# Performance work log

Measured on AMD Instinct MI355X. Metric: run time of the kernel, lower is better.

The kernel has to match this reference:

```python
import jax, jax.numpy as jnp
import numpy as np

K = 8        # number of nearest neighbors (idw default)
POWER = 2    # inverse-distance power (idw default)
EPS = 1e-8


def setup_inputs() -> dict:
    key = jax.random.key(0)
    kq, kr, kf = jax.random.split(key, 3)
    N, M = 32768, 16384
    # scale coords so points are spread out like real LiDAR scenes
    query_points = jax.random.normal(kq, (N, 3), dtype=jnp.float32) * 10.0
    ref_points = jax.random.normal(kr, (M, 3), dtype=jnp.float32) * 10.0
    ref_flow = jax.random.normal(kf, (M, 3), dtype=jnp.float32)
    return {"query_points": query_points, "ref_points": ref_points, "ref_flow": ref_flow}


def reference(query_points, ref_points, ref_flow):
    # cdist: Euclidean distance [N, M] via (q-r)^2 = |q|^2 + |r|^2 - 2 q.r
    q2 = jnp.sum(query_points * query_points, axis=-1, keepdims=True)      # [N,1]
    r2 = jnp.sum(ref_points * ref_points, axis=-1)                          # [M]
    d2 = q2 + r2 - 2.0 * (query_points @ ref_points.T)                      # [N,M]
    dist = jnp.sqrt(jnp.maximum(d2, 0.0))
    # k smallest distances == top_k of negated distances
    neg_knn, knn_idx = jax.lax.top_k(-dist, K)                               # [N,K]
    knn_dist = -neg_knn
    # inverse-distance weights: 1 / (d^power + eps), normalized over k
    weights = 1.0 / (knn_dist ** POWER + EPS)
    weights = weights / jnp.sum(weights, axis=1, keepdims=True)
    knn_flow = ref_flow[knn_idx]                                             # [N,K,3]
    return jnp.sum(weights[..., None] * knn_flow, axis=1)                    # [N,3]
```

## Files before the change

kernel.cpp:

```cpp
#include <hip/hip_runtime.h>

#define KNN    8
#define BLOCK  256
#define TILE   2048
#define GD     32
#define NC     (GD*GD*GD)
#define EPSW   1e-8f
#define BIGF   3.4e38f

__device__ __forceinline__ void insert8(float d2, int j, float bd[KNN], int bi[KNN]) {
    if (d2 < bd[0]) {
        bd[0] = d2; bi[0] = j;
#pragma unroll
        for (int t = 0; t < KNN - 1; t++) {
            if (bd[t] < bd[t + 1]) {
                float td = bd[t]; bd[t] = bd[t + 1]; bd[t + 1] = td;
                int   ti = bi[t]; bi[t] = bi[t + 1]; bi[t + 1] = ti;
            }
        }
    }
}

__device__ __forceinline__ void ced(float& a, int& ai, float& b, int& bi) {
    if (a < b) { float t = a; a = b; b = t; int ti = ai; ai = bi; bi = ti; }
}
__device__ __forceinline__ void sort8_desc(float d[KNN], int ix[KNN]) {
    ced(d[0],ix[0],d[4],ix[4]); ced(d[1],ix[1],d[5],ix[5]);
    ced(d[2],ix[2],d[6],ix[6]); ced(d[3],ix[3],d[7],ix[7]);
    ced(d[0],ix[0],d[2],ix[2]); ced(d[1],ix[1],d[3],ix[3]);
    ced(d[4],ix[4],d[6],ix[6]); ced(d[5],ix[5],d[7],ix[7]);
    ced(d[0],ix[0],d[1],ix[1]); ced(d[2],ix[2],d[3],ix[3]);
    ced(d[4],ix[4],d[5],ix[5]); ced(d[6],ix[6],d[7],ix[7]);
}
__device__ __forceinline__ void merge_lists(float bd[KNN], int bi[KNN], int mask, bool sort_after) {
    float pd[KNN]; int pi[KNN];
#pragma unroll
    for (int j = 0; j < KNN; j++) { pd[j] = __shfl_xor(bd[j], mask); pi[j] = __shfl_xor(bi[j], mask); }
#pragma unroll
    for (int j = 0; j < KNN; j++) {
        if (pd[KNN - 1 - j] < bd[j]) { bd[j] = pd[KNN - 1 - j]; bi[j] = pi[KNN - 1 - j]; }
    }
    if (sort_after) sort8_desc(bd, bi);
}
__device__ __forceinline__ float merged_thr4(const float bd[KNN]) {
    float c[KNN], p[KNN];
#pragma unroll
    for (int j = 0; j < KNN; j++) c[j] = bd[j];
#pragma unroll
    for (int j = 0; j < KNN; j++) p[j] = __shfl_xor(c[j], 1);
#pragma unroll
    for (int j = 0; j < KNN; j++) c[j] = fminf(c[j], p[KNN - 1 - j]);
    {
        float mx, mn;
        mx = fmaxf(c[0],c[4]); mn = fminf(c[0],c[4]); c[0]=mx; c[4]=mn;
        mx = fmaxf(c[1],c[5]); mn = fminf(c[1],c[5]); c[1]=mx; c[5]=mn;
        mx = fmaxf(c[2],c[6]); mn = fminf(c[2],c[6]); c[2]=mx; c[6]=mn;
        mx = fmaxf(c[3],c[7]); mn = fminf(c[3],c[7]); c[3]=mx; c[7]=mn;
        mx = fmaxf(c[0],c[2]); mn = fminf(c[0],c[2]); c[0]=mx; c[2]=mn;
        mx = fmaxf(c[1],c[3]); mn = fminf(c[1],c[3]); c[1]=mx; c[3]=mn;
        mx = fmaxf(c[4],c[6]); mn = fminf(c[4],c[6]); c[4]=mx; c[6]=mn;
        mx = fmaxf(c[5],c[7]); mn = fminf(c[5],c[7]); c[5]=mx; c[7]=mn;
        mx = fmaxf(c[0],c[1]); mn = fminf(c[0],c[1]); c[0]=mx; c[1]=mn;
        mx = fmaxf(c[2],c[3]); mn = fminf(c[2],c[3]); c[2]=mx; c[3]=mn;
        mx = fmaxf(c[4],c[5]); mn = fminf(c[4],c[5]); c[4]=mx; c[5]=mn;
        mx = fmaxf(c[6],c[7]); mn = fminf(c[6],c[7]); c[6]=mx; c[7]=mn;
    }
#pragma unroll
    for (int j = 0; j < KNN; j++) p[j] = __shfl_xor(c[j], 2);
#pragma unroll
    for (int j = 0; j < KNN; j++) c[j] = fminf(c[j], p[KNN - 1 - j]);
    float m = c[0];
#pragma unroll
    for (int j = 1; j < KNN; j++) m = fmaxf(m, c[j]);
    return m;
}

__device__ __forceinline__ unsigned fenc(float f) {
    unsigned u = __float_as_uint(f);
    return (u & 0x80000000u) ? ~u : (u | 0x80000000u);
}
__device__ __forceinline__ float fdec(unsigned e) {
    unsigned u = (e & 0x80000000u) ? (e ^ 0x80000000u) : ~e;
    return __uint_as_float(u);
}

__device__ __forceinline__ void load_bb(const unsigned* __restrict__ bbw,
                                        float mn[3], float inv[3], float& hmin) {
    hmin = BIGF;
#pragma unroll
    for (int a = 0; a < 3; a++) {
        float lo = fdec(bbw[a]), hi = fdec(bbw[3 + a]);
        float w = fmaxf(hi - lo, 1e-9f);
        mn[a] = lo;
        inv[a] = (float)GD / w;
        hmin = fminf(hmin, w / (float)GD);
    }
}

__device__ __forceinline__ int cell_clamp(int c) {
    return c < 0 ? 0 : (c > GD - 1 ? GD - 1 : c);
}


__global__ __launch_bounds__(256) void bbox_atomic(const float* __restrict__ r, int M,
                                                   unsigned* __restrict__ bbw) {
    float mn0 = BIGF, mn1 = BIGF, mn2 = BIGF;
    float mx0 = -BIGF, mx1 = -BIGF, mx2 = -BIGF;
    for (int j = blockIdx.x * 256 + threadIdx.x; j < M; j += gridDim.x * 256) {
        float x = r[3 * j], y = r[3 * j + 1], z = r[3 * j + 2];
        mn0 = fminf(mn0, x); mx0 = fmaxf(mx0, x);
        mn1 = fminf(mn1, y); mx1 = fmaxf(mx1, y);
        mn2 = fminf(mn2, z); mx2 = fmaxf(mx2, z);
    }
#pragma unroll
    for (int o = 32; o > 0; o >>= 1) {
        mn0 = fminf(mn0, __shfl_xor(mn0, o));
        mn1 = fminf(mn1, __shfl_xor(mn1, o));
        mn2 = fminf(mn2, __shfl_xor(mn2, o));
        mx0 = fmaxf(mx0, __shfl_xor(mx0, o));
        mx1 = fmaxf(mx1, __shfl_xor(mx1, o));
        mx2 = fmaxf(mx2, __shfl_xor(mx2, o));
    }
    if ((threadIdx.x & 63) == 0) {
        atomicMin(bbw + 0, fenc(mn0)); atomicMin(bbw + 1, fenc(mn1)); atomicMin(bbw + 2, fenc(mn2));
        atomicMax(bbw + 3, fenc(mx0)); atomicMax(bbw + 4, fenc(mx1)); atomicMax(bbw + 5, fenc(mx2));
    }
}

__global__ __launch_bounds__(256) void hist2(const float* __restrict__ r,
                                             const float* __restrict__ q,
                                             int M, int N, const unsigned* __restrict__ bbw,
                                             int* __restrict__ rcid, int* __restrict__ qcid,
                                             int* __restrict__ rcnt, int* __restrict__ qcnt) {
    float mn[3], inv[3], hmin;
    load_bb(bbw, mn, inv, hmin);
    int i = blockIdx.x * 256 + threadIdx.x;
    if (i < M) {
        int cx = cell_clamp((int)((r[3 * i]     - mn[0]) * inv[0]));
        int cy = cell_clamp((int)((r[3 * i + 1] - mn[1]) * inv[1]));
        int cz = cell_clamp((int)((r[3 * i + 2] - mn[2]) * inv[2]));
        int cid = (cz * GD + cy) * GD + cx;
        rcid[i] = cid;
        atomicAdd(rcnt + cid, 1);
    } else if (i < M + N) {
        int j = i - M;
        int cx = cell_clamp((int)((q[3 * j]     - mn[0]) * inv[0]));
        int cy = cell_clamp((int)((q[3 * j + 1] - mn[1]) * inv[1]));
        int cz = cell_clamp((int)((q[3 * j + 2] - mn[2]) * inv[2]));
        int cid = (cz * GD + cy) * GD + cx;
        qcid[j] = cid;
        atomicAdd(qcnt + cid, 1);
    }
}

__global__ __launch_bounds__(1024) void scan2(int* __restrict__ rcnt, int* __restrict__ rstart,
                                              int* __restrict__ qcnt, int* __restrict__ qstart) {
    int* cnt = (blockIdx.x == 0) ? rcnt : qcnt;
    int* st  = (blockIdx.x == 0) ? rstart : qstart;
    __shared__ int part[1024];
    int t = threadIdx.x;
    int base = t * 32;
    int s = 0;
#pragma unroll
    for (int k = 0; k < 32; k++) s += cnt[base + k];
    part[t] = s;
    __syncthreads();
    for (int off = 1; off < 1024; off <<= 1) {
        int v = (t >= off) ? part[t - off] : 0;
        __syncthreads();
        part[t] += v;
        __syncthreads();
    }
    int run = part[t] - s;
#pragma unroll
    for (int k = 0; k < 32; k++) {
        int c = cnt[base + k];
        st[base + k] = run;
        cnt[base + k] = run;
        run += c;
    }
    if (t == 1023) st[NC] = run;
}

__global__ __launch_bounds__(256) void scatter2(const float* __restrict__ r, int M, int N,
                                                const int* __restrict__ rcid,
                                                const int* __restrict__ qcid,
                                                int* __restrict__ rcur, int* __restrict__ qcur,
                                                float4* __restrict__ rps, int* __restrict__ sidx,
                                                int* __restrict__ qorder) {
    int i = blockIdx.x * 256 + threadIdx.x;
    if (i < M) {
        int pos = atomicAdd(rcur + rcid[i], 1);
        float x = r[3 * i], y = r[3 * i + 1], z = r[3 * i + 2];
        rps[pos] = make_float4(x, y, z, x * x + y * y + z * z);
        sidx[pos] = i;
    } else if (i < M + N) {
        int j = i - M;
        int pos = atomicAdd(qcur + qcid[j], 1);
        qorder[pos] = j;
    }
}

__global__ __launch_bounds__(256) void knn_pass1(
    const float4* __restrict__ rps, const int* __restrict__ rstart,
    const int* __restrict__ qorder, const float* __restrict__ q,
    const int* __restrict__ sidx, const float* __restrict__ f,
    const unsigned* __restrict__ bbw, float* __restrict__ out,
    int* __restrict__ pend, int* __restrict__ pcnt, int N) {
    int t = blockIdx.x * 256 + threadIdx.x;
    int g = t >> 2;
    int sub = t & 3;
    if (g >= N) return;
    int qi = qorder[g];
    float qx = q[3 * qi], qy = q[3 * qi + 1], qz = q[3 * qi + 2];
    float q2 = qx * qx + qy * qy + qz * qz;
    float mn[3], inv[3], hmin;
    load_bb(bbw, mn, inv, hmin);
    int cx = cell_clamp((int)((qx - mn[0]) * inv[0]));
    int cy = cell_clamp((int)((qy - mn[1]) * inv[1]));
    int cz = cell_clamp((int)((qz - mn[2]) * inv[2]));

    float bd[KNN]; int bi[KNN];
#pragma unroll
    for (int k = 0; k < KNN; k++) { bd[k] = BIGF; bi[k] = 0; }
    float thr = BIGF;

    int rs[9], re[9];
#pragma unroll
    for (int dz = -1; dz <= 1; dz++) {
#pragma unroll
        for (int dy = -1; dy <= 1; dy++) {
            int k = (dz + 1) * 3 + (dy + 1);
            int z = cz + dz, y = cy + dy;
            if ((unsigned)z >= GD || (unsigned)y >= GD) { rs[k] = 0; re[k] = 0; }
            else {
                int rowb = (z * GD + y) * GD;
                int x0 = max(cx - 1, 0), x1 = min(cx + 1, GD - 1);
                rs[k] = rstart[rowb + x0]; re[k] = rstart[rowb + x1 + 1];
            }
        }
    }
#pragma unroll
    for (int k = 0; k < 9; k++) {
        for (int ii = rs[k] + sub; ii < re[k]; ii += 4) {
            float4 p = rps[ii];
            float d2 = (q2 + p.w) - 2.0f * (qx * p.x + qy * p.y + qz * p.z);
            if (d2 < thr) { insert8(d2, ii, bd, bi); thr = bd[0]; }
        }
    }
    float mthr = merged_thr4(bd);
    thr = fminf(thr, mthr);
    bool done = (mthr <= hmin * hmin);

    if (!done) {
        for (int dz = -2; dz <= 2; dz++) {
            int z = cz + dz;
            if ((unsigned)z >= GD) continue;
            for (int dy = -2; dy <= 2; dy++) {
                int y = cy + dy;
                if ((unsigned)y >= GD) continue;
                int rowb = (z * GD + y) * GD;
                if (dz == -2 || dz == 2 || dy == -2 || dy == 2) {
                    int x0 = max(cx - 2, 0), x1 = min(cx + 2, GD - 1);
                    int s = rstart[rowb + x0], e = rstart[rowb + x1 + 1];
                    for (int ii = s + sub; ii < e; ii += 4) {
                        float4 p = rps[ii];
                        float d2 = (q2 + p.w) - 2.0f * (qx * p.x + qy * p.y + qz * p.z);
                        if (d2 < thr) { insert8(d2, ii, bd, bi); thr = bd[0]; }
                    }
                } else {
                    int xl = cx - 2, xr = cx + 2;
                    if (xl >= 0) {
                        int s = rstart[rowb + xl], e = rstart[rowb + xl + 1];
                        for (int ii = s + sub; ii < e; ii += 4) {
                            float4 p = rps[ii];
                            float d2 = (q2 + p.w) - 2.0f * (qx * p.x + qy * p.y + qz * p.z);
                            if (d2 < thr) { insert8(d2, ii, bd, bi); thr = bd[0]; }
                        }
                    }
                    if (xr < GD) {
                        int s = rstart[rowb + xr], e = rstart[rowb + xr + 1];
                        for (int ii = s + sub; ii < e; ii += 4) {
                            float4 p = rps[ii];
                            float d2 = (q2 + p.w) - 2.0f * (qx * p.x + qy * p.y + qz * p.z);
                            if (d2 < thr) { insert8(d2, ii, bd, bi); thr = bd[0]; }
                        }
                    }
                }
            }
        }
        mthr = merged_thr4(bd);
        done = (mthr <= 4.0f * hmin * hmin);
    }

    if (!done) {
        if (sub == 0) { int pos = atomicAdd(pcnt, 1); pend[pos] = qi; }
        return;
    }

    merge_lists(bd, bi, 1, true);
    merge_lists(bd, bi, 2, false);
    if (sub == 0) {
        float wsum = 0.f, ox = 0.f, oy = 0.f, oz = 0.f;
#pragma unroll
        for (int k = 0; k < KNN; k++) {
            float w = 1.0f / (fmaxf(bd[k], 0.0f) + EPSW);
            int j = sidx[bi[k]];
            wsum += w;
            ox += w * f[3 * j];
            oy += w * f[3 * j + 1];
            oz += w * f[3 * j + 2];
        }
        float invw = 1.0f / wsum;
        out[3 * qi]     = ox * invw;
        out[3 * qi + 1] = oy * invw;
        out[3 * qi + 2] = oz * invw;
    }
}

__global__ __launch_bounds__(256) void knn_pass2(
    const float4* __restrict__ rps, const int* __restrict__ pend,
    const int* __restrict__ pcnt, const float* __restrict__ q,
    const int* __restrict__ sidx, const float* __restrict__ f,
    float* __restrict__ out, int M) {
    int lane = threadIdx.x & 63;
    int wid = (blockIdx.x * 256 + threadIdx.x) >> 6;
    int nw = gridDim.x * 4;
    int cnt = *pcnt;
    for (int w = wid; w < cnt; w += nw) {
        int qi = pend[w];
        float qx = q[3 * qi], qy = q[3 * qi + 1], qz = q[3 * qi + 2];
        float q2 = qx * qx + qy * qy + qz * qz;
        float bd[KNN]; int bi[KNN];
#pragma unroll
        for (int k = 0; k < KNN; k++) { bd[k] = BIGF; bi[k] = 0; }
        float thr = BIGF;
        int i = lane;
        for (; i + 192 < M; i += 256) {
            float4 p0 = rps[i];
            float4 p1 = rps[i + 64];
            float4 p2 = rps[i + 128];
            float4 p3 = rps[i + 192];
            float d0 = (q2 + p0.w) - 2.0f * (qx * p0.x + qy * p0.y + qz * p0.z);
            float d1 = (q2 + p1.w) - 2.0f * (qx * p1.x + qy * p1.y + qz * p1.z);
            float d2 = (q2 + p2.w) - 2.0f * (qx * p2.x + qy * p2.y + qz * p2.z);
            float d3 = (q2 + p3.w) - 2.0f * (qx * p3.x + qy * p3.y + qz * p3.z);
            if (d0 < thr) { insert8(d0, i,       bd, bi); thr = bd[0]; }
            if (d1 < thr) { insert8(d1, i + 64,  bd, bi); thr = bd[0]; }
            if (d2 < thr) { insert8(d2, i + 128, bd, bi); thr = bd[0]; }
            if (d3 < thr) { insert8(d3, i + 192, bd, bi); thr = bd[0]; }
        }
        for (; i < M; i += 64) {
            float4 p = rps[i];
            float d2 = (q2 + p.w) - 2.0f * (qx * p.x + qy * p.y + qz * p.z);
            if (d2 < thr) { insert8(d2, i, bd, bi); thr = bd[0]; }
        }
        merge_lists(bd, bi, 1, true);
        merge_lists(bd, bi, 2, true);
        merge_lists(bd, bi, 4, true);
        merge_lists(bd, bi, 8, true);
        merge_lists(bd, bi, 16, true);
        merge_lists(bd, bi, 32, false);
        if (lane == 0) {
            float wsum = 0.f, ox = 0.f, oy = 0.f, oz = 0.f;
#pragma unroll
            for (int k = 0; k < KNN; k++) {
                float wgt = 1.0f / (fmaxf(bd[k], 0.0f) + EPSW);
                int j = sidx[bi[k]];
                wsum += wgt;
                ox += wgt * f[3 * j];
                oy += wgt * f[3 * j + 1];
                oz += wgt * f[3 * j + 2];
            }
            float invw = 1.0f / wsum;
            out[3 * qi]     = ox * invw;
            out[3 * qi + 1] = oy * invw;
            out[3 * qi + 2] = oz * invw;
        }
    }
}

__global__ __launch_bounds__(BLOCK) void knn_fused(
    const float* __restrict__ q, const float* __restrict__ r,
    const float* __restrict__ f, float* __restrict__ out, int N, int M) {
    __shared__ float4 lds[TILE];
    int qi = blockIdx.x * BLOCK + threadIdx.x;
    float qx = 0.f, qy = 0.f, qz = 0.f, q2 = 0.f;
    if (qi < N) {
        qx = q[3 * qi]; qy = q[3 * qi + 1]; qz = q[3 * qi + 2];
        q2 = qx * qx + qy * qy + qz * qz;
    }
    float bd[KNN]; int bi[KNN];
#pragma unroll
    for (int k = 0; k < KNN; k++) { bd[k] = BIGF; bi[k] = 0; }
    for (int tb = 0; tb < M; tb += TILE) {
        int cnt = min(TILE, M - tb);
        for (int i = threadIdx.x; i < cnt; i += BLOCK) {
            int j = tb + i;
            float rx = r[3 * j], ry = r[3 * j + 1], rz = r[3 * j + 2];
            lds[i] = make_float4(rx, ry, rz, rx * rx + ry * ry + rz * rz);
        }
        __syncthreads();
        for (int i = 0; i < cnt; i++) {
            float4 p = lds[i];
            float d2 = (q2 + p.w) - 2.0f * (qx * p.x + qy * p.y + qz * p.z);
            insert8(d2, tb + i, bd, bi);
        }
        __syncthreads();
    }
    if (qi < N) {
        float wsum = 0.f, ox = 0.f, oy = 0.f, oz = 0.f;
#pragma unroll
        for (int k = 0; k < KNN; k++) {
            float w = 1.0f / (fmaxf(bd[k], 0.0f) + EPSW);
            int j = bi[k];
            ox += w * f[3 * j];
            oy += w * f[3 * j + 1];
            oz += w * f[3 * j + 2];
        }
        float inv = 1.0f / wsum;
        out[3 * qi]     = ox * inv;
        out[3 * qi + 1] = oy * inv;
        out[3 * qi + 2] = oz * inv;
    }
}

extern "C" void kernel_launch(void* const* d_in, const int* in_sizes, int n_in,
                              void* d_out, int out_size, void* d_ws, size_t ws_size,
                              hipStream_t stream) {
    const float* q = (const float*)d_in[0];
    const float* r = (const float*)d_in[1];
    const float* f = (const float*)d_in[2];
    float* out = (float*)d_out;
    int N = in_sizes[0] / 3;
    int M = in_sizes[1] / 3;

    size_t off = 0;
    auto take = [&](size_t b) { size_t o = off; off += (b + 255) & ~(size_t)255; return o; };
    size_t o_rps  = take((size_t)M * 16);
    size_t o_sidx = take((size_t)M * 4);
    size_t o_rcid = take((size_t)M * 4);
    size_t o_qcid = take((size_t)N * 4);
    size_t o_qord = take((size_t)N * 4);
    size_t o_rst  = take((size_t)(NC + 1) * 4);
    size_t o_qst  = take((size_t)(NC + 1) * 4);
    size_t o_rcur = take((size_t)NC * 4);
    size_t o_qcur = take((size_t)NC * 4);
    size_t o_pcnt = take(4);
    size_t o_pend = take((size_t)N * 4);
    size_t o_bb   = take(64);

    int grid_x = (N + BLOCK - 1) / BLOCK;
    if (off <= ws_size) {
        char* w = (char*)d_ws;
        float4* rps   = (float4*)(w + o_rps);
        int* sidx     = (int*)(w + o_sidx);
        int* rcid     = (int*)(w + o_rcid);
        int* qcid     = (int*)(w + o_qcid);
        int* qorder   = (int*)(w + o_qord);
        int* rstart   = (int*)(w + o_rst);
        int* qstart   = (int*)(w + o_qst);
        int* rcur     = (int*)(w + o_rcur);
        int* qcur     = (int*)(w + o_qcur);
        int* pcnt     = (int*)(w + o_pcnt);
        int* pend     = (int*)(w + o_pend);
        unsigned* bbw = (unsigned*)(w + o_bb);

        hipMemsetAsync(w + o_rcur, 0, o_pcnt + 4 - o_rcur, stream);
        hipMemsetAsync(w + o_bb, 0xFF, 12, stream);
        hipMemsetAsync(w + o_bb + 12, 0x00, 12, stream);

        int g_all = (M + N + 255) / 256;
        bbox_atomic<<<64, 256, 0, stream>>>(r, M, bbw);
        hist2<<<g_all, 256, 0, stream>>>(r, q, M, N, bbw, rcid, qcid, rcur, qcur);
        scan2<<<2, 1024, 0, stream>>>(rcur, rstart, qcur, qstart);
        scatter2<<<g_all, 256, 0, stream>>>(r, M, N, rcid, qcid, rcur, qcur, rps, sidx, qorder);
        int g_p1 = (int)(((size_t)N * 4 + 255) / 256);
        knn_pass1<<<g_p1, 256, 0, stream>>>(rps, rstart, qorder, q, sidx, f, bbw, out,
                                            pend, pcnt, N);
        knn_pass2<<<512, 256, 0, stream>>>(rps, pend, pcnt, q, sidx, f, out, M);
    } else {
        knn_fused<<<grid_x, BLOCK, 0, stream>>>(q, r, f, out, N, M);
    }
}
```

Before: 225.6 us.

## Add radius-3 shell search, block-wide brute fallback, fold memsets into bbox kernel

Adds a third grid shell (radius 3) before falling back to brute force, so fewer queries reach the costly full scan. The fallback pass now assigns one 256-thread block per pending query instead of one wave, and merges the four per-wave top-8 lists through shared memory. It also replaces two memsets with zeroing inside the bbox kernel and stores the max as a negated min, so a single 0xFF memset initialises all bounds. The costs are more per-query branching and code size in pass1, plus block barriers in pass2.

```diff
diff --git a/kernel.cpp b/kernel.cpp
--- a/kernel.cpp
+++ b/kernel.cpp
@@ -89,7 +89,7 @@
     hmin = BIGF;
 #pragma unroll
     for (int a = 0; a < 3; a++) {
-        float lo = fdec(bbw[a]), hi = fdec(bbw[3 + a]);
+        float lo = fdec(bbw[a]), hi = -fdec(bbw[3 + a]);
         float w = fmaxf(hi - lo, 1e-9f);
         mn[a] = lo;
         inv[a] = (float)GD / w;
@@ -102,11 +102,14 @@
 }
 
 
-__global__ __launch_bounds__(256) void bbox_atomic(const float* __restrict__ r, int M,
-                                                   unsigned* __restrict__ bbw) {
+__global__ __launch_bounds__(256) void bbox_zero(const float* __restrict__ r, int M,
+                                                 unsigned* __restrict__ bbw,
+                                                 int* __restrict__ zbase, int zcount) {
+    int idx = blockIdx.x * 256 + threadIdx.x;
+    for (int j = idx; j < zcount; j += gridDim.x * 256) zbase[j] = 0;
     float mn0 = BIGF, mn1 = BIGF, mn2 = BIGF;
     float mx0 = -BIGF, mx1 = -BIGF, mx2 = -BIGF;
-    for (int j = blockIdx.x * 256 + threadIdx.x; j < M; j += gridDim.x * 256) {
+    for (int j = idx; j < M; j += gridDim.x * 256) {
         float x = r[3 * j], y = r[3 * j + 1], z = r[3 * j + 2];
         mn0 = fminf(mn0, x); mx0 = fmaxf(mx0, x);
         mn1 = fminf(mn1, y); mx1 = fmaxf(mx1, y);
@@ -123,7 +126,7 @@
     }
     if ((threadIdx.x & 63) == 0) {
         atomicMin(bbw + 0, fenc(mn0)); atomicMin(bbw + 1, fenc(mn1)); atomicMin(bbw + 2, fenc(mn2));
-        atomicMax(bbw + 3, fenc(mx0)); atomicMax(bbw + 4, fenc(mx1)); atomicMax(bbw + 5, fenc(mx2));
+        atomicMin(bbw + 3, fenc(-mx0)); atomicMin(bbw + 4, fenc(-mx1)); atomicMin(bbw + 5, fenc(-mx2));
     }
 }
 
@@ -201,6 +204,49 @@
     }
 }
 
+__device__ __forceinline__ void scan_shell(
+    int R, int cx, int cy, int cz, int sub,
+    const float4* __restrict__ rps, const int* __restrict__ rstart,
+    float qx, float qy, float qz, float q2,
+    float bd[KNN], int bi[KNN], float& thr) {
+    for (int dz = -R; dz <= R; ++dz) {
+        int z = cz + dz;
+        if ((unsigned)z >= GD) continue;
+        for (int dy = -R; dy <= R; ++dy) {
+            int y = cy + dy;
+            if ((unsigned)y >= GD) continue;
+            int rowb = (z * GD + y) * GD;
+            if (dz == -R || dz == R || dy == -R || dy == R) {
+                int x0 = max(cx - R, 0), x1 = min(cx + R, GD - 1);
+                int s = rstart[rowb + x0], e = rstart[rowb + x1 + 1];
+                for (int ii = s + sub; ii < e; ii += 4) {
+                    float4 p = rps[ii];
+                    float d2 = (q2 + p.w) - 2.0f * (qx * p.x + qy * p.y + qz * p.z);
+                    if (d2 < thr) { insert8(d2, ii, bd, bi); thr = bd[0]; }
+                }
+            } else {
+                int xl = cx - R, xr = cx + R;
+                if (xl >= 0) {
+                    int s = rstart[rowb + xl], e = rstart[rowb + xl + 1];
+                    for (int ii = s + sub; ii < e; ii += 4) {
+                        float4 p = rps[ii];
+                        float d2 = (q2 + p.w) - 2.0f * (qx * p.x + qy * p.y + qz * p.z);
+                        if (d2 < thr) { insert8(d2, ii, bd, bi); thr = bd[0]; }
+                    }
+                }
+                if (xr < GD) {
+                    int s = rstart[rowb + xr], e = rstart[rowb + xr + 1];
+                    for (int ii = s + sub; ii < e; ii += 4) {
+                        float4 p = rps[ii];
+                        float d2 = (q2 + p.w) - 2.0f * (qx * p.x + qy * p.y + qz * p.z);
+                        if (d2 < thr) { insert8(d2, ii, bd, bi); thr = bd[0]; }
+                    }
+                }
+            }
+        }
+    }
+}
+
 __global__ __launch_bounds__(256) void knn_pass1(
     const float4* __restrict__ rps, const int* __restrict__ rstart,
     const int* __restrict__ qorder, const float* __restrict__ q,
@@ -253,44 +299,15 @@
     bool done = (mthr <= hmin * hmin);
 
     if (!done) {
-        for (int dz = -2; dz <= 2; dz++) {
-            int z = cz + dz;
-            if ((unsigned)z >= GD) continue;
-            for (int dy = -2; dy <= 2; dy++) {
-                int y = cy + dy;
-                if ((unsigned)y >= GD) continue;
-                int rowb = (z * GD + y) * GD;
-                if (dz == -2 || dz == 2 || dy == -2 || dy == 2) {
-                    int x0 = max(cx - 2, 0), x1 = min(cx + 2, GD - 1);
-                    int s = rstart[rowb + x0], e = rstart[rowb + x1 + 1];
-                    for (int ii = s + sub; ii < e; ii += 4) {
-                        float4 p = rps[ii];
-                        float d2 = (q2 + p.w) - 2.0f * (qx * p.x + qy * p.y + qz * p.z);
-                        if (d2 < thr) { insert8(d2, ii, bd, bi); thr = bd[0]; }
-                    }
-                } else {
-                    int xl = cx - 2, xr = cx + 2;
-                    if (xl >= 0) {
-                        int s = rstart[rowb + xl], e = rstart[rowb + xl + 1];
-                        for (int ii = s + sub; ii < e; ii += 4) {
-                            float4 p = rps[ii];
-                            float d2 = (q2 + p.w) - 2.0f * (qx * p.x + qy * p.y + qz * p.z);
-                            if (d2 < thr) { insert8(d2, ii, bd, bi); thr = bd[0]; }
-                        }
-                    }
-                    if (xr < GD) {
-                        int s = rstart[rowb + xr], e = rstart[rowb + xr + 1];
-                        for (int ii = s + sub; ii < e; ii += 4) {
-                            float4 p = rps[ii];
-                            float d2 = (q2 + p.w) - 2.0f * (qx * p.x + qy * p.y + qz * p.z);
-                            if (d2 < thr) { insert8(d2, ii, bd, bi); thr = bd[0]; }
-                        }
-                    }
-                }
-            }
-        }
+        scan_shell(2, cx, cy, cz, sub, rps, rstart, qx, qy, qz, q2, bd, bi, thr);
         mthr = merged_thr4(bd);
+        thr = fminf(thr, mthr);
         done = (mthr <= 4.0f * hmin * hmin);
+    }
+    if (!done) {
+        scan_shell(3, cx, cy, cz, sub, rps, rstart, qx, qy, qz, q2, bd, bi, thr);
+        mthr = merged_thr4(bd);
+        done = (mthr <= 9.0f * hmin * hmin);
     }
 
     if (!done) {
@@ -323,11 +340,12 @@
     const int* __restrict__ pcnt, const float* __restrict__ q,
     const int* __restrict__ sidx, const float* __restrict__ f,
     float* __restrict__ out, int M) {
-    int lane = threadIdx.x & 63;
-    int wid = (blockIdx.x * 256 + threadIdx.x) >> 6;
-    int nw = gridDim.x * 4;
+    __shared__ float sd[4][KNN];
+    __shared__ int   si[4][KNN];
+    int tid = threadIdx.x;
+    int lane = tid & 63, wv = tid >> 6;
     int cnt = *pcnt;
-    for (int w = wid; w < cnt; w += nw) {
+    for (int w = blockIdx.x; w < cnt; w += gridDim.x) {
         int qi = pend[w];
         float qx = q[3 * qi], qy = q[3 * qi + 1], qz = q[3 * qi + 2];
         float q2 = qx * qx + qy * qy + qz * qz;
@@ -335,22 +353,34 @@
 #pragma unroll
         for (int k = 0; k < KNN; k++) { bd[k] = BIGF; bi[k] = 0; }
         float thr = BIGF;
-        int i = lane;
-        for (; i + 192 < M; i += 256) {
+        int i = tid;
+        for (; i + 1792 < M; i += 2048) {
             float4 p0 = rps[i];
-            float4 p1 = rps[i + 64];
-            float4 p2 = rps[i + 128];
-            float4 p3 = rps[i + 192];
+            float4 p1 = rps[i + 256];
+            float4 p2 = rps[i + 512];
+            float4 p3 = rps[i + 768];
+            float4 p4 = rps[i + 1024];
+            float4 p5 = rps[i + 1280];
+            float4 p6 = rps[i + 1536];
+            float4 p7 = rps[i + 1792];
             float d0 = (q2 + p0.w) - 2.0f * (qx * p0.x + qy * p0.y + qz * p0.z);
             float d1 = (q2 + p1.w) - 2.0f * (qx * p1.x + qy * p1.y + qz * p1.z);
             float d2 = (q2 + p2.w) - 2.0f * (qx * p2.x + qy * p2.y + qz * p2.z);
             float d3 = (q2 + p3.w) - 2.0f * (qx * p3.x + qy * p3.y + qz * p3.z);
-            if (d0 < thr) { insert8(d0, i,       bd, bi); thr = bd[0]; }
-            if (d1 < thr) { insert8(d1, i + 64,  bd, bi); thr = bd[0]; }
-            if (d2 < thr) { insert8(d2, i + 128, bd, bi); thr = bd[0]; }
-            if (d3 < thr) { insert8(d3, i + 192, bd, bi); thr = bd[0]; }
-        }
-        for (; i < M; i += 64) {
+            float d4 = (q2 + p4.w) - 2.0f * (qx * p4.x + qy * p4.y + qz * p4.z);
+            float d5 = (q2 + p5.w) - 2.0f * (qx * p5.x + qy * p5.y + qz * p5.z);
+            float d6 = (q2 + p6.w) - 2.0f * (qx * p6.x + qy * p6.y + qz * p6.z);
+            float d7 = (q2 + p7.w) - 2.0f * (qx * p7.x + qy * p7.y + qz * p7.z);
+            if (d0 < thr) { insert8(d0, i,        bd, bi); thr = bd[0]; }
+            if (d1 < thr) { insert8(d1, i + 256,  bd, bi); thr = bd[0]; }
+            if (d2 < thr) { insert8(d2, i + 512,  bd, bi); thr = bd[0]; }
+            if (d3 < thr) { insert8(d3, i + 768,  bd, bi); thr = bd[0]; }
+            if (d4 < thr) { insert8(d4, i + 1024, bd, bi); thr = bd[0]; }
+            if (d5 < thr) { insert8(d5, i + 1280, bd, bi); thr = bd[0]; }
+            if (d6 < thr) { insert8(d6, i + 1536, bd, bi); thr = bd[0]; }
+            if (d7 < thr) { insert8(d7, i + 1792, bd, bi); thr = bd[0]; }
+        }
+        for (; i < M; i += 256) {
             float4 p = rps[i];
             float d2 = (q2 + p.w) - 2.0f * (qx * p.x + qy * p.y + qz * p.z);
             if (d2 < thr) { insert8(d2, i, bd, bi); thr = bd[0]; }
@@ -360,8 +390,17 @@
         merge_lists(bd, bi, 4, true);
         merge_lists(bd, bi, 8, true);
         merge_lists(bd, bi, 16, true);
-        merge_lists(bd, bi, 32, false);
+        merge_lists(bd, bi, 32, true);
         if (lane == 0) {
+#pragma unroll
+            for (int k = 0; k < KNN; k++) { sd[wv][k] = bd[k]; si[wv][k] = bi[k]; }
+        }
+        __syncthreads();
+        if (tid == 0) {
+            for (int v = 1; v < 4; v++) {
+#pragma unroll
+                for (int k = 0; k < KNN; k++) insert8(sd[v][k], si[v][k], bd, bi);
+            }
             float wsum = 0.f, ox = 0.f, oy = 0.f, oz = 0.f;
 #pragma unroll
             for (int k = 0; k < KNN; k++) {
@@ -377,6 +416,7 @@
             out[3 * qi + 1] = oy * invw;
             out[3 * qi + 2] = oz * invw;
         }
+        __syncthreads();
     }
 }
 
@@ -466,12 +506,11 @@
         int* pend     = (int*)(w + o_pend);
         unsigned* bbw = (unsigned*)(w + o_bb);
 
-        hipMemsetAsync(w + o_rcur, 0, o_pcnt + 4 - o_rcur, stream);
-        hipMemsetAsync(w + o_bb, 0xFF, 12, stream);
-        hipMemsetAsync(w + o_bb + 12, 0x00, 12, stream);
-
+        hipMemsetAsync(w + o_bb, 0xFF, 24, stream);
+
+        int zcount = (int)((o_pcnt + 4 - o_rcur) / 4);
         int g_all = (M + N + 255) / 256;
-        bbox_atomic<<<64, 256, 0, stream>>>(r, M, bbw);
+        bbox_zero<<<64, 256, 0, stream>>>(r, M, bbw, rcur, zcount);
         hist2<<<g_all, 256, 0, stream>>>(r, q, M, N, bbw, rcid, qcid, rcur, qcur);
         scan2<<<2, 1024, 0, stream>>>(rcur, rstart, qcur, qstart);
         scatter2<<<g_all, 256, 0, stream>>>(r, M, N, rcid, qcid, rcur, qcur, rps, sidx, qorder);
```

New measurement: 202.5 us. -10.3%, faster.
